# Kernel tuning notes

Hardware: AMD Instinct MI355X
Metric: run time of the kernel (lower is better)

Reference implementation:

```python
import jax, jax.numpy as jnp
import numpy as np

R = 16
LORA_ALPHA = 16.0
SCALING = LORA_ALPHA / R  # = 1.0, matches lora_alpha / r


def setup_inputs() -> dict:
    key = jax.random.key(0)
    k_x, k_a, k_a0, k_b = jax.random.split(key, 4)
    d, r, n_tok = 4096, R, 8192
    inv_sqrt_d = 1.0 / np.sqrt(d)
    x = jax.random.normal(k_x, (n_tok, d), dtype=jnp.float32)
    # mode='standard': A0 ~ N(0, 1/d), B0 = 0; A, B initialized as clones of A0, B0
    A0 = jax.random.normal(k_a0, (r, d), dtype=jnp.float32) * inv_sqrt_d
    B0 = jnp.zeros((d, r), dtype=jnp.float32)
    # perturb A, B slightly to emulate trained params (still faithful math)
    A = A0 + jax.random.normal(k_a, (r, d), dtype=jnp.float32) * inv_sqrt_d
    B = B0 + jax.random.normal(k_b, (d, r), dtype=jnp.float32) * inv_sqrt_d
    return {"x": x, "A": A, "B": B, "A0": A0, "B0": B0}


def reference(x, A, B, A0, B0):
    # Faithful to torch: dW = (B @ A - B0 @ A0) * scaling; out = x @ dW
    # (mode='standard' uses the offset-subtracted delta)
    dW = (B @ A - B0 @ A0) * SCALING          # [d, d]
    return x @ dW                              # [N, d]
```

## Files before the change

kernel.cpp:

```cpp
#include <hip/hip_runtime.h>

#define N_TOK 8192
#define D     4096
#define RLO   16
#define R2    32
#define KSL   16

typedef __bf16  bf16x8  __attribute__((ext_vector_type(8)));
typedef short   short8v __attribute__((ext_vector_type(8)));
typedef float   f32x4   __attribute__((ext_vector_type(4)));

__device__ __forceinline__ short bf1(float f) {
  __bf16 b = (__bf16)f;
  return __builtin_bit_cast(short, b);
}

__device__ __forceinline__ short8v cvt8(float4 lo, float4 hi) {
  bf16x8 b;
  b[0] = (__bf16)lo.x; b[1] = (__bf16)lo.y; b[2] = (__bf16)lo.z; b[3] = (__bf16)lo.w;
  b[4] = (__bf16)hi.x; b[5] = (__bf16)hi.y; b[6] = (__bf16)hi.z; b[7] = (__bf16)hi.w;
  return __builtin_bit_cast(short8v, b);
}


__global__ __launch_bounds__(256) void prep_kernel(
    const float* __restrict__ A, const float* __restrict__ B,
    const float* __restrict__ A0, const float* __restrict__ B0,
    ushort* __restrict__ PTb, ushort* __restrict__ Qpk) {
  int idx = blockIdx.x * 256 + threadIdx.x;
  int r = idx >> 12;
  int k = idx & (D - 1);
  float pt, q;
  if (r < RLO) {
    pt = B[k * RLO + r];
    q  = A[r * D + k];
  } else {
    pt = -B0[k * RLO + (r - RLO)];
    q  = A0[(r - RLO) * D + k];
  }
  PTb[idx] = (ushort)bf1(pt);
  Qpk[(size_t)k * R2 + r] = (ushort)bf1(q);
}

__global__ __launch_bounds__(256) void s1_kernel(
    const float* __restrict__ x, const ushort* __restrict__ PTb,
    float* __restrict__ UP) {
  const int tid  = threadIdx.x;
  const int w    = tid >> 6;
  const int lane = tid & 63;
  const int l16  = lane & 15;
  const int kg   = lane >> 4;
  const int rowblk = blockIdx.x & 255;
  const int kout   = blockIdx.x >> 8;
  const int row0 = rowblk * 32;
  const int kb   = kout * 1024 + w * 256 + kg * 8;

  const float*  xp0 = x   + (size_t)(row0 + l16) * D + kb;
  const float*  xp1 = xp0 + (size_t)16 * D;
  const ushort* pb0 = PTb + (size_t)l16 * D + kb;
  const ushort* pb1 = pb0 + (size_t)16 * D;

  f32x4 acc00 = {0.f, 0.f, 0.f, 0.f};
  f32x4 acc01 = {0.f, 0.f, 0.f, 0.f};
  f32x4 acc10 = {0.f, 0.f, 0.f, 0.f};
  f32x4 acc11 = {0.f, 0.f, 0.f, 0.f};

#pragma unroll
  for (int s = 0; s < 8; ++s) {
    const int ko = s * 32;
    const float4 a0l = *(const float4*)(xp0 + ko);
    const float4 a0h = *(const float4*)(xp0 + ko + 4);
    const float4 a1l = *(const float4*)(xp1 + ko);
    const float4 a1h = *(const float4*)(xp1 + ko + 4);
    const short8v b0 = *(const short8v*)(pb0 + ko);
    const short8v b1 = *(const short8v*)(pb1 + ko);
    const short8v a0 = cvt8(a0l, a0h);
    const short8v a1 = cvt8(a1l, a1h);
    acc00 = __builtin_amdgcn_mfma_f32_16x16x32_bf16(a0, b0, acc00, 0, 0, 0);
    acc01 = __builtin_amdgcn_mfma_f32_16x16x32_bf16(a0, b1, acc01, 0, 0, 0);
    acc10 = __builtin_amdgcn_mfma_f32_16x16x32_bf16(a1, b0, acc10, 0, 0, 0);
    acc11 = __builtin_amdgcn_mfma_f32_16x16x32_bf16(a1, b1, acc11, 0, 0, 0);
  }

  float* up = UP + ((size_t)(kout * 4 + w) * N_TOK + row0) * R2;
#pragma unroll
  for (int j = 0; j < 4; ++j) {
    up[(kg * 4 + j) * R2 + l16]             = acc00[j];
    up[(kg * 4 + j) * R2 + 16 + l16]        = acc01[j];
    up[(16 + kg * 4 + j) * R2 + l16]        = acc10[j];
    up[(16 + kg * 4 + j) * R2 + 16 + l16]   = acc11[j];
  }
}

__global__ __launch_bounds__(256) void s2_kernel(
    const float* __restrict__ UP, const ushort* __restrict__ Qpk,
    float* __restrict__ out) {
  __shared__ __align__(16) ushort usb[32][R2];
  const int tid = threadIdx.x;
  const int rowblk = (int)blockIdx.x >> 2;
  const int jseg   = blockIdx.x & 3;
  const int row0 = rowblk * 32;

  {
    const int row = tid >> 3;
    const int r4  = (tid & 7) * 4;
    float4 s = make_float4(0.f, 0.f, 0.f, 0.f);
#pragma unroll
    for (int ks = 0; ks < KSL; ++ks) {
      const float4 v = *(const float4*)(UP + ((size_t)ks * N_TOK + row0 + row) * R2 + r4);
      s.x += v.x; s.y += v.y; s.z += v.z; s.w += v.w;
    }
    usb[row][r4 + 0] = (ushort)bf1(s.x);
    usb[row][r4 + 1] = (ushort)bf1(s.y);
    usb[row][r4 + 2] = (ushort)bf1(s.z);
    usb[row][r4 + 3] = (ushort)bf1(s.w);
  }
  __syncthreads();

  const int w    = tid >> 6;
  const int lane = tid & 63;
  const int l16  = lane & 15;
  const int kg   = lane >> 4;
  const int jbase = jseg * 1024 + w * 256;

  const short8v ua0 = *(const short8v*)&usb[l16][kg * 8];
  const short8v ua1 = *(const short8v*)&usb[16 + l16][kg * 8];
  const f32x4 z = {0.f, 0.f, 0.f, 0.f};

#pragma unroll
  for (int jt = 0; jt < 16; ++jt) {
    const int j = jbase + jt * 16 + l16;
    const short8v qb = *(const short8v*)(Qpk + (size_t)j * R2 + kg * 8);
    const f32x4 d0 = __builtin_amdgcn_mfma_f32_16x16x32_bf16(ua0, qb, z, 0, 0, 0);
    const f32x4 d1 = __builtin_amdgcn_mfma_f32_16x16x32_bf16(ua1, qb, z, 0, 0, 0);
    float* o = out + (size_t)(row0 + kg * 4) * D + j;
#pragma unroll
    for (int jr = 0; jr < 4; ++jr) {
      o[(size_t)jr * D]        = d0[jr];
      o[(size_t)(16 + jr) * D] = d1[jr];
    }
  }
}

extern "C" void kernel_launch(void* const* d_in, const int* in_sizes, int n_in,
                              void* d_out, int out_size, void* d_ws, size_t ws_size,
                              hipStream_t stream) {
  const float* x  = (const float*)d_in[0];
  const float* A  = (const float*)d_in[1];
  const float* B  = (const float*)d_in[2];
  const float* A0 = (const float*)d_in[3];
  const float* B0 = (const float*)d_in[4];
  float* out = (float*)d_out;

  ushort* PTb = (ushort*)d_ws;
  ushort* Qpk = PTb + (size_t)R2 * D;
  float*  UP  = (float*)(Qpk + (size_t)D * R2);

  hipLaunchKernelGGL(prep_kernel, dim3((R2 * D) / 256), dim3(256), 0, stream,
                     A, B, A0, B0, PTb, Qpk);
  hipLaunchKernelGGL(s1_kernel, dim3(1024), dim3(256), 0, stream,
                     x, PTb, UP);
  hipLaunchKernelGGL(s2_kernel, dim3(1024), dim3(256), 0, stream,
                     UP, Qpk, out);
}
```

Baseline: 80.00 us.

## Reduce full-K partials inside s1 blocks via shared memory instead of split-K buffer

The s1 kernel now gives each block 16 token rows over the full 4096-wide K, with each wave covering a quarter of K. The four wave partials are reduced through shared memory, and the finished u is written once. This removes the 16-way split-K partial buffer and its re-read and summation in s2, which cuts global traffic and work in s2. In exchange s1 runs fewer, longer blocks, and each wave loops 32 times with a single x row tile, which lowers B-fragment reuse and parallelism.

```diff
diff --git a/kernel.cpp b/kernel.cpp
--- a/kernel.cpp
+++ b/kernel.cpp
@@ -4,7 +4,6 @@
 #define D     4096
 #define RLO   16
 #define R2    32
-#define KSL   16
 
 typedef __bf16  bf16x8  __attribute__((ext_vector_type(8)));
 typedef short   short8v __attribute__((ext_vector_type(8)));
@@ -44,56 +43,55 @@
 
 __global__ __launch_bounds__(256) void s1_kernel(
     const float* __restrict__ x, const ushort* __restrict__ PTb,
-    float* __restrict__ UP) {
+    float* __restrict__ u) {
+  __shared__ float red[4][16][R2 + 2];
   const int tid  = threadIdx.x;
   const int w    = tid >> 6;
   const int lane = tid & 63;
   const int l16  = lane & 15;
   const int kg   = lane >> 4;
-  const int rowblk = blockIdx.x & 255;
-  const int kout   = blockIdx.x >> 8;
-  const int row0 = rowblk * 32;
-  const int kb   = kout * 1024 + w * 256 + kg * 8;
+  const int row0 = blockIdx.x * 16;
+  const int kb   = w * 1024 + kg * 8;
 
-  const float*  xp0 = x   + (size_t)(row0 + l16) * D + kb;
-  const float*  xp1 = xp0 + (size_t)16 * D;
+  const float*  xp = x   + (size_t)(row0 + l16) * D + kb;
   const ushort* pb0 = PTb + (size_t)l16 * D + kb;
   const ushort* pb1 = pb0 + (size_t)16 * D;
 
-  f32x4 acc00 = {0.f, 0.f, 0.f, 0.f};
-  f32x4 acc01 = {0.f, 0.f, 0.f, 0.f};
-  f32x4 acc10 = {0.f, 0.f, 0.f, 0.f};
-  f32x4 acc11 = {0.f, 0.f, 0.f, 0.f};
+  f32x4 acc0 = {0.f, 0.f, 0.f, 0.f};
+  f32x4 acc1 = {0.f, 0.f, 0.f, 0.f};
 
 #pragma unroll
-  for (int s = 0; s < 8; ++s) {
+  for (int s = 0; s < 32; ++s) {
     const int ko = s * 32;
-    const float4 a0l = *(const float4*)(xp0 + ko);
-    const float4 a0h = *(const float4*)(xp0 + ko + 4);
-    const float4 a1l = *(const float4*)(xp1 + ko);
-    const float4 a1h = *(const float4*)(xp1 + ko + 4);
+    const float4 alo = *(const float4*)(xp + ko);
+    const float4 ahi = *(const float4*)(xp + ko + 4);
     const short8v b0 = *(const short8v*)(pb0 + ko);
     const short8v b1 = *(const short8v*)(pb1 + ko);
-    const short8v a0 = cvt8(a0l, a0h);
-    const short8v a1 = cvt8(a1l, a1h);
-    acc00 = __builtin_amdgcn_mfma_f32_16x16x32_bf16(a0, b0, acc00, 0, 0, 0);
-    acc01 = __builtin_amdgcn_mfma_f32_16x16x32_bf16(a0, b1, acc01, 0, 0, 0);
-    acc10 = __builtin_amdgcn_mfma_f32_16x16x32_bf16(a1, b0, acc10, 0, 0, 0);
-    acc11 = __builtin_amdgcn_mfma_f32_16x16x32_bf16(a1, b1, acc11, 0, 0, 0);
+    const short8v a  = cvt8(alo, ahi);
+    acc0 = __builtin_amdgcn_mfma_f32_16x16x32_bf16(a, b0, acc0, 0, 0, 0);
+    acc1 = __builtin_amdgcn_mfma_f32_16x16x32_bf16(a, b1, acc1, 0, 0, 0);
   }
 
-  float* up = UP + ((size_t)(kout * 4 + w) * N_TOK + row0) * R2;
 #pragma unroll
   for (int j = 0; j < 4; ++j) {
-    up[(kg * 4 + j) * R2 + l16]             = acc00[j];
-    up[(kg * 4 + j) * R2 + 16 + l16]        = acc01[j];
-    up[(16 + kg * 4 + j) * R2 + l16]        = acc10[j];
-    up[(16 + kg * 4 + j) * R2 + 16 + l16]   = acc11[j];
+    red[w][kg * 4 + j][l16]      = acc0[j];
+    red[w][kg * 4 + j][16 + l16] = acc1[j];
+  }
+  __syncthreads();
+
+#pragma unroll
+  for (int half = 0; half < 2; ++half) {
+    const int idx = half * 256 + tid;
+    const int row = idx >> 5;
+    const int r   = idx & 31;
+    const float s = red[0][row][r] + red[1][row][r] +
+                    red[2][row][r] + red[3][row][r];
+    u[(size_t)(row0 + row) * R2 + r] = s;
   }
 }
 
 __global__ __launch_bounds__(256) void s2_kernel(
-    const float* __restrict__ UP, const ushort* __restrict__ Qpk,
+    const float* __restrict__ u, const ushort* __restrict__ Qpk,
     float* __restrict__ out) {
   __shared__ __align__(16) ushort usb[32][R2];
   const int tid = threadIdx.x;
@@ -104,16 +102,11 @@
   {
     const int row = tid >> 3;
     const int r4  = (tid & 7) * 4;
-    float4 s = make_float4(0.f, 0.f, 0.f, 0.f);
-#pragma unroll
-    for (int ks = 0; ks < KSL; ++ks) {
-      const float4 v = *(const float4*)(UP + ((size_t)ks * N_TOK + row0 + row) * R2 + r4);
-      s.x += v.x; s.y += v.y; s.z += v.z; s.w += v.w;
-    }
-    usb[row][r4 + 0] = (ushort)bf1(s.x);
-    usb[row][r4 + 1] = (ushort)bf1(s.y);
-    usb[row][r4 + 2] = (ushort)bf1(s.z);
-    usb[row][r4 + 3] = (ushort)bf1(s.w);
+    const float4 v = *(const float4*)(u + (size_t)(row0 + row) * R2 + r4);
+    usb[row][r4 + 0] = (ushort)bf1(v.x);
+    usb[row][r4 + 1] = (ushort)bf1(v.y);
+    usb[row][r4 + 2] = (ushort)bf1(v.z);
+    usb[row][r4 + 3] = (ushort)bf1(v.w);
   }
   __syncthreads();
 
@@ -154,12 +147,12 @@
 
   ushort* PTb = (ushort*)d_ws;
   ushort* Qpk = PTb + (size_t)R2 * D;
-  float*  UP  = (float*)(Qpk + (size_t)D * R2);
+  float*  u   = (float*)(Qpk + (size_t)D * R2);
 
   hipLaunchKernelGGL(prep_kernel, dim3((R2 * D) / 256), dim3(256), 0, stream,
                      A, B, A0, B0, PTb, Qpk);
-  hipLaunchKernelGGL(s1_kernel, dim3(1024), dim3(256), 0, stream,
-                     x, PTb, UP);
-  hipLaunchKernelGGL(s2_kernel, dim3(1024), dim3(256), 0, stream,
-                     UP, Qpk, out);
+  hipLaunchKernelGGL(s1_kernel, dim3(N_TOK / 16), dim3(256), 0, stream,
+                     x, PTb, u);
+  hipLaunchKernelGGL(s2_kernel, dim3((N_TOK / 32) * 4), dim3(256), 0, stream,
+                     u, Qpk, out);
 }
```

Result: faster. 66.68 us (-16.6%).
